# Optimization experiments

Hardware: AMD Instinct MI355X
Metric: run time of the kernel (lower is better)

Reference implementation:

```python
import jax, jax.numpy as jnp
import numpy as np

T, H, NH, NKV, HD = 2048, 1024, 16, 4, 64
I, E, TOPK = 2048, 8, 2
EPS = 1e-5
ROPE_BASE = 10000.0


def rms_norm(x, w):
    var = jnp.mean(x * x, axis=-1, keepdims=True)
    return x * jax.lax.rsqrt(var + EPS) * w


def apply_rope(x, positions, n_heads):
    # neox-style rotary over full head_dim
    t = x.reshape(-1, n_heads, HD)
    half = HD // 2
    inv_freq = 1.0 / (ROPE_BASE ** (jnp.arange(0, half, dtype=jnp.float32) / half))
    freqs = positions.astype(jnp.float32)[:, None] * inv_freq[None, :]  # [T, half]
    cos = jnp.cos(freqs)[:, None, :]
    sin = jnp.sin(freqs)[:, None, :]
    x1, x2 = t[..., :half], t[..., half:]
    rot = jnp.concatenate([x1 * cos - x2 * sin, x2 * cos + x1 * sin], axis=-1)
    return rot.reshape(x.shape)


def setup_inputs():
    key = jax.random.key(0)
    ks = jax.random.split(key, 9)
    s = 0.02
    return dict(
        positions=jnp.arange(T, dtype=jnp.int32),
        hidden_states=jax.random.normal(ks[0], (T, H), jnp.float32),
        input_ln_w=jnp.ones((H,), jnp.float32),
        post_ln_w=jnp.ones((H,), jnp.float32),
        residual_ln_w=jnp.ones((H,), jnp.float32),
        qkv_w=jax.random.normal(ks[1], ((NH + 2 * NKV) * HD, H), jnp.float32) * s,
        o_w=jax.random.normal(ks[2], (H, NH * HD), jnp.float32) * s,
        gate_w=jax.random.normal(ks[3], (E, H), jnp.float32) * s,
        ws=jax.random.normal(ks[4], (E, 2 * I, H), jnp.float32) * s,
        w2s=jax.random.normal(ks[5], (E, H, I), jnp.float32) * s,
        res_w13=jax.random.normal(ks[6], (2 * H, H), jnp.float32) * s,
        res_w2=jax.random.normal(ks[7], (H, H), jnp.float32) * s,
    )


def attention(x, positions, qkv_w, o_w):
    qkv = x @ qkv_w.T  # [T, (NH+2*NKV)*HD]
    q, k, v = jnp.split(qkv, [NH * HD, NH * HD + NKV * HD], axis=-1)
    q = apply_rope(q, positions, NH)
    k = apply_rope(k, positions, NKV)
    q = q.reshape(T, NH, HD)
    k = k.reshape(T, NKV, HD)
    v = v.reshape(T, NKV, HD)
    rep = NH // NKV  # GQA: repeat kv heads
    k = jnp.repeat(k, rep, axis=1)
    v = jnp.repeat(v, rep, axis=1)
    scale = HD ** -0.5
    scores = jnp.einsum('tnd,snd->nts', q, k) * scale  # [NH, T, T]
    causal = jnp.tril(jnp.ones((T, T), dtype=bool))
    scores = jnp.where(causal[None], scores, -jnp.inf)
    probs = jax.nn.softmax(scores, axis=-1)
    out = jnp.einsum('nts,snd->tnd', probs, v).reshape(T, NH * HD)
    return out @ o_w.T


def silu_and_mul(gu):
    g, u = jnp.split(gu, 2, axis=-1)
    return jax.nn.silu(g) * u


def moe(x, gate_w, ws, w2s):
    logits = x @ gate_w.T  # [T, E]
    probs = jax.nn.softmax(logits, axis=-1)
    topk_w, topk_ids = jax.lax.top_k(probs, TOPK)
    topk_w = topk_w / jnp.sum(topk_w, axis=-1, keepdims=True)  # renormalize (top_k > 1)
    routes = jnp.zeros((x.shape[0], E), x.dtype).at[
        jnp.arange(x.shape[0])[:, None], topk_ids].set(topk_w)  # [T, E] sparse routing
    gu = jnp.einsum('th,eih->tei', x, ws)        # [T, E, 2I]
    act = silu_and_mul(gu)                        # [T, E, I]
    eo = jnp.einsum('tei,ehi->teh', act, w2s)     # [T, E, H]
    return jnp.einsum('te,teh->th', routes, eo)


def reference(positions, hidden_states, input_ln_w, post_ln_w, residual_ln_w,
              qkv_w, o_w, gate_w, ws, w2s, res_w13, res_w2):
    residual_input = hidden_states
    h = rms_norm(hidden_states, input_ln_w)
    h = attention(h, positions, qkv_w, o_w)
    residual_attn = residual_input + h
    # parallel residual MLP branch (ffn_dim == hidden)
    r = rms_norm(residual_attn, residual_ln_w)
    r = silu_and_mul(r @ res_w13.T) @ res_w2.T
    residual_mlp = residual_attn + r
    # MoE branch
    m = rms_norm(residual_attn, post_ln_w)
    m = moe(m, gate_w, ws, w2s)
    return residual_mlp + m
```

## Files before the change

kernel.cpp:

```cpp
#include <hip/hip_runtime.h>
#include <stdint.h>


typedef _Float16 f16;
typedef _Float16 f16x8 __attribute__((ext_vector_type(8)));
typedef _Float16 f16x4 __attribute__((ext_vector_type(4)));
typedef float f32x4 __attribute__((ext_vector_type(4)));

#define DEV __device__ __forceinline__

DEV void glds16(const void* g, void* l) {
  __builtin_amdgcn_global_load_lds((const __attribute__((address_space(1))) void*)g,
                                   (__attribute__((address_space(3))) void*)l, 16, 0, 0);
}

__global__ void cvt_f16_kernel(const float* __restrict__ in, f16* __restrict__ outp) {
  const size_t i = ((size_t)blockIdx.x * 256 + threadIdx.x) * 4;
  float4 f = *(const float4*)(in + i);
  f16x4 o;
  o[0] = (f16)f.x; o[1] = (f16)f.y; o[2] = (f16)f.z; o[3] = (f16)f.w;
  *(f16x4*)(outp + i) = o;
}

__global__ void cvt_f16x2_kernel(const float* __restrict__ in,
                                 f16* __restrict__ oh, f16* __restrict__ ol) {
  const size_t i = ((size_t)blockIdx.x * 256 + threadIdx.x) * 4;
  float4 f = *(const float4*)(in + i);
  f16x4 h, l;
  h[0] = (f16)f.x; l[0] = (f16)(f.x - (float)h[0]);
  h[1] = (f16)f.y; l[1] = (f16)(f.y - (float)h[1]);
  h[2] = (f16)f.z; l[2] = (f16)(f.z - (float)h[2]);
  h[3] = (f16)f.w; l[3] = (f16)(f.w - (float)h[3]);
  *(f16x4*)(oh + i) = h;
  *(f16x4*)(ol + i) = l;
}

__global__ void rmsnorm_kernel(const float* __restrict__ in, const float* __restrict__ w,
                               f16* __restrict__ outp) {
  const int t = blockIdx.x * 4 + (threadIdx.x >> 6);
  const int lane = threadIdx.x & 63;
  const float* x = in + (size_t)t * 1024;
  float v[16]; float ss = 0.f;
#pragma unroll
  for (int j = 0; j < 16; j++) { float a = x[lane + 64 * j]; v[j] = a; ss += a * a; }
#pragma unroll
  for (int m = 1; m < 64; m <<= 1) ss += __shfl_xor(ss, m);
  const float rs = rsqrtf(ss * (1.f / 1024.f) + 1e-5f);
#pragma unroll
  for (int j = 0; j < 16; j++)
    outp[(size_t)t * 1024 + lane + 64 * j] = (f16)(v[j] * rs * w[lane + 64 * j]);
}

__global__ void rmsnorm_dual_kernel(const float* __restrict__ in,
                                    const float* __restrict__ w1, const float* __restrict__ w2,
                                    f16* __restrict__ o1, f16* __restrict__ o2) {
  const int t = blockIdx.x * 4 + (threadIdx.x >> 6);
  const int lane = threadIdx.x & 63;
  const float* x = in + (size_t)t * 1024;
  float v[16]; float ss = 0.f;
#pragma unroll
  for (int j = 0; j < 16; j++) { float a = x[lane + 64 * j]; v[j] = a; ss += a * a; }
#pragma unroll
  for (int m = 1; m < 64; m <<= 1) ss += __shfl_xor(ss, m);
  const float rs = rsqrtf(ss * (1.f / 1024.f) + 1e-5f);
#pragma unroll
  for (int j = 0; j < 16; j++) {
    float nv = v[j] * rs;
    size_t idx = (size_t)t * 1024 + lane + 64 * j;
    o1[idx] = (f16)(nv * w1[lane + 64 * j]);
    o2[idx] = (f16)(nv * w2[lane + 64 * j]);
  }
}

template <int EPI, int BN, int SPLITK = 1>
__global__ __launch_bounds__(256) void gemm_f16_kernel(
    const f16* __restrict__ A, const f16* __restrict__ B,
    void* __restrict__ outp, const float* __restrict__ addsrc,
    int M, int N, int K) {
  constexpr int JT = BN / 32;
  constexpr int L = (BN == 128) ? 4 : 3;
  __shared__ __attribute__((aligned(16))) f16 As[4][128 * 32];
  __shared__ __attribute__((aligned(16))) f16 Bs[4][BN * 32];
  const int tid = threadIdx.x;
  const size_t row0 = (size_t)blockIdx.y * 128, col0 = (size_t)blockIdx.x * BN;
  const int ks = (SPLITK > 1) ? (int)blockIdx.z : 0;
  const int kspan = K / SPLITK, kb = ks * kspan;
  const int nt = kspan >> 5;
  const int c0 = tid, c1 = tid + 256;
  const int sw0 = ((c0 & 3) ^ ((c0 >> 3) & 3)) * 8;
  const int sw1 = ((c1 & 3) ^ ((c1 >> 3) & 3)) * 8;
  const f16* a0 = A + (row0 + (c0 >> 2)) * K + sw0;
  const f16* a1 = A + (row0 + (c1 >> 2)) * K + sw1;
  const f16* b0 = B + (col0 + (c0 >> 2)) * K + sw0;
  const f16* b1 = B + (col0 + ((BN == 128) ? (c1 >> 2) : 0)) * K + ((BN == 128) ? sw1 : 0);

  const int wave = tid >> 6, lane = tid & 63, lr = lane >> 4, lc = lane & 15;
  const int wr = wave >> 1, wc = wave & 1;
  const int rsw = (lr ^ ((lc >> 1) & 3)) * 8;

  f32x4 acc[4][JT];
#pragma unroll
  for (int i = 0; i < 4; i++)
#pragma unroll
    for (int j = 0; j < JT; j++) acc[i][j] = (f32x4){0.f, 0.f, 0.f, 0.f};

  auto stage = [&](int k0, int buf) {
    glds16(a0 + k0, As[buf] + c0 * 8);
    glds16(a1 + k0, As[buf] + c1 * 8);
    glds16(b0 + k0, Bs[buf] + c0 * 8);
    if constexpr (BN == 128) glds16(b1 + k0, Bs[buf] + c1 * 8);
  };

  stage(kb, 0); stage(kb + 32, 1); stage(kb + 64, 2);
  for (int t = 0; t < nt; ++t) {
    if (t <= nt - 3)      asm volatile("s_waitcnt vmcnt(%0)" :: "n"(2 * L) : "memory");
    else if (t == nt - 2) asm volatile("s_waitcnt vmcnt(%0)" :: "n"(L) : "memory");
    else                  asm volatile("s_waitcnt vmcnt(0)" ::: "memory");
    __builtin_amdgcn_s_barrier();
    asm volatile("" ::: "memory");
    if (t + 3 < nt) stage(kb + (t + 3) * 32, (t + 3) & 3);
    const f16* Ab = As[t & 3];
    const f16* Bb = Bs[t & 3];
    f16x8 af[4], bfr[JT];
#pragma unroll
    for (int i = 0; i < 4; i++)
      af[i] = *(const f16x8*)(Ab + (wr * 64 + i * 16 + lc) * 32 + rsw);
#pragma unroll
    for (int j = 0; j < JT; j++)
      bfr[j] = *(const f16x8*)(Bb + (wc * (BN / 2) + j * 16 + lc) * 32 + rsw);
#pragma unroll
    for (int i = 0; i < 4; i++)
#pragma unroll
      for (int j = 0; j < JT; j++)
        acc[i][j] = __builtin_amdgcn_mfma_f32_16x16x32_f16(af[i], bfr[j], acc[i][j], 0, 0, 0);
  }

#pragma unroll
  for (int i = 0; i < 4; i++)
#pragma unroll
    for (int j = 0; j < JT; j++) {
      const size_t rbase = row0 + wr * 64 + i * 16 + lr * 4;
      const size_t col = col0 + wc * (BN / 2) + j * 16 + lc;
#pragma unroll
      for (int r = 0; r < 4; r++) {
        size_t idx = (rbase + r) * N + col;
        if constexpr (SPLITK > 1) {
          ((float*)outp)[(size_t)ks * M * N + idx] = acc[i][j][r];
        } else if constexpr (EPI == 0) ((float*)outp)[idx] = acc[i][j][r];
        else if constexpr (EPI == 1) ((float*)outp)[idx] = acc[i][j][r] + addsrc[idx];
        else ((f16*)outp)[idx] = (f16)acc[i][j][r];
      }
    }
}

template <int SPLITK>
__global__ __launch_bounds__(256) void gemm_f16x2_add_kernel(
    const f16* __restrict__ Ah, const f16* __restrict__ Al,
    const f16* __restrict__ Bh, const f16* __restrict__ Bl,
    float* __restrict__ outp, const float* __restrict__ addsrc,
    int M, int N, int K) {
  __shared__ __attribute__((aligned(16))) f16 Ash[3][128 * 32];
  __shared__ __attribute__((aligned(16))) f16 Asl[3][128 * 32];
  __shared__ __attribute__((aligned(16))) f16 Bsh[3][64 * 32];
  __shared__ __attribute__((aligned(16))) f16 Bsl[3][64 * 32];
  const int tid = threadIdx.x;
  const size_t row0 = (size_t)blockIdx.y * 128, col0 = (size_t)blockIdx.x * 64;
  const int ks = (SPLITK > 1) ? (int)blockIdx.z : 0;
  const int kspan = K / SPLITK, kb = ks * kspan;
  const int nt = kspan >> 5;
  const int c0 = tid, c1 = tid + 256;
  const int sw0 = ((c0 & 3) ^ ((c0 >> 3) & 3)) * 8;
  const int sw1 = ((c1 & 3) ^ ((c1 >> 3) & 3)) * 8;
  const size_t aoff0 = (row0 + (c0 >> 2)) * K + sw0;
  const size_t aoff1 = (row0 + (c1 >> 2)) * K + sw1;
  const size_t boff0 = (col0 + (c0 >> 2)) * K + sw0;

  const int wave = tid >> 6, lane = tid & 63, lr = lane >> 4, lc = lane & 15;
  const int wr = wave >> 1, wc = wave & 1;
  const int rsw = (lr ^ ((lc >> 1) & 3)) * 8;

  f32x4 acc[4][2];
#pragma unroll
  for (int i = 0; i < 4; i++)
#pragma unroll
    for (int j = 0; j < 2; j++) acc[i][j] = (f32x4){0.f, 0.f, 0.f, 0.f};

  auto stage = [&](int k0, int buf) {
    glds16(Ah + aoff0 + k0, Ash[buf] + c0 * 8);
    glds16(Ah + aoff1 + k0, Ash[buf] + c1 * 8);
    glds16(Al + aoff0 + k0, Asl[buf] + c0 * 8);
    glds16(Al + aoff1 + k0, Asl[buf] + c1 * 8);
    glds16(Bh + boff0 + k0, Bsh[buf] + c0 * 8);
    glds16(Bl + boff0 + k0, Bsl[buf] + c0 * 8);
  };

  stage(kb, 0); stage(kb + 32, 1);
  int bc = 0, bs = 2;
  for (int t = 0; t < nt; ++t) {
    if (t <= nt - 2) asm volatile("s_waitcnt vmcnt(%0)" :: "n"(6) : "memory");
    else             asm volatile("s_waitcnt vmcnt(0)" ::: "memory");
    __builtin_amdgcn_s_barrier();
    asm volatile("" ::: "memory");
    if (t + 2 < nt) stage(kb + (t + 2) * 32, bs);
    f16x8 afh[4], afl[4], bfh[2], bfl[2];
#pragma unroll
    for (int i = 0; i < 4; i++) {
      const int ro = (wr * 64 + i * 16 + lc) * 32 + rsw;
      afh[i] = *(const f16x8*)(Ash[bc] + ro);
      afl[i] = *(const f16x8*)(Asl[bc] + ro);
    }
#pragma unroll
    for (int j = 0; j < 2; j++) {
      const int ro = (wc * 32 + j * 16 + lc) * 32 + rsw;
      bfh[j] = *(const f16x8*)(Bsh[bc] + ro);
      bfl[j] = *(const f16x8*)(Bsl[bc] + ro);
    }
#pragma unroll
    for (int i = 0; i < 4; i++)
#pragma unroll
      for (int j = 0; j < 2; j++) {
        acc[i][j] = __builtin_amdgcn_mfma_f32_16x16x32_f16(afh[i], bfh[j], acc[i][j], 0, 0, 0);
        acc[i][j] = __builtin_amdgcn_mfma_f32_16x16x32_f16(afh[i], bfl[j], acc[i][j], 0, 0, 0);
        acc[i][j] = __builtin_amdgcn_mfma_f32_16x16x32_f16(afl[i], bfh[j], acc[i][j], 0, 0, 0);
      }
    bc = (bc == 2) ? 0 : bc + 1;
    bs = (bs == 2) ? 0 : bs + 1;
  }

#pragma unroll
  for (int i = 0; i < 4; i++)
#pragma unroll
    for (int j = 0; j < 2; j++) {
      const size_t rbase = row0 + wr * 64 + i * 16 + lr * 4;
      const size_t col = col0 + wc * 32 + j * 16 + lc;
#pragma unroll
      for (int r = 0; r < 4; r++) {
        size_t idx = (rbase + r) * N + col;
        if constexpr (SPLITK > 1) outp[(size_t)ks * M * N + idx] = acc[i][j][r];
        else outp[idx] = acc[i][j][r] + addsrc[idx];
      }
    }
}

template <int DIVROW, int BN, int SPLITK = 1>
__global__ __launch_bounds__(256) void gemm_moe_kernel(
    const f16* __restrict__ A, const f16* __restrict__ Ball, void* __restrict__ outp,
    const int* __restrict__ perm, const int* __restrict__ counts,
    int N, int K, size_t strideB) {
  constexpr int JT = BN / 32;
  constexpr int L = (BN == 128) ? 4 : 3;
  const int e = (int)blockIdx.z / SPLITK;
  const int ks = (int)blockIdx.z % SPLITK;
  const int cnt = counts[e];
  const int bm = blockIdx.y;
  if (bm * 128 >= cnt) return;
  const int kspan = K / SPLITK, kb = ks * kspan;
  const int nt = kspan >> 5;
  const f16* B = Ball + (size_t)e * strideB;
  __shared__ __attribute__((aligned(16))) f16 As[4][128 * 32];
  __shared__ __attribute__((aligned(16))) f16 Bs[4][BN * 32];
  const int tid = threadIdx.x;
  const size_t col0 = (size_t)blockIdx.x * BN;
  const int c0 = tid, c1 = tid + 256;
  const int pbase = e * 2048 + bm * 128;
  const int rt0 = c0 >> 2, rt1 = c1 >> 2;
  const int sid0 = (bm * 128 + rt0 < cnt) ? perm[pbase + rt0] : 0;
  const int sid1 = (bm * 128 + rt1 < cnt) ? perm[pbase + rt1] : 0;
  const size_t ar0 = DIVROW ? (size_t)(sid0 >> 1) : (size_t)sid0;
  const size_t ar1 = DIVROW ? (size_t)(sid1 >> 1) : (size_t)sid1;
  const int sw0 = ((c0 & 3) ^ ((c0 >> 3) & 3)) * 8;
  const int sw1 = ((c1 & 3) ^ ((c1 >> 3) & 3)) * 8;
  const f16* ap0 = A + ar0 * K + sw0;
  const f16* ap1 = A + ar1 * K + sw1;
  const f16* b0 = B + (col0 + (c0 >> 2)) * K + sw0;
  const f16* b1 = B + (col0 + ((BN == 128) ? (c1 >> 2) : 0)) * K + ((BN == 128) ? sw1 : 0);

  const int wave = tid >> 6, lane = tid & 63, lr = lane >> 4, lc = lane & 15;
  const int wr = wave >> 1, wc = wave & 1;
  const int rsw = (lr ^ ((lc >> 1) & 3)) * 8;

  f32x4 acc[4][JT];
#pragma unroll
  for (int i = 0; i < 4; i++)
#pragma unroll
    for (int j = 0; j < JT; j++) acc[i][j] = (f32x4){0.f, 0.f, 0.f, 0.f};

  auto stage = [&](int k0, int buf) {
    glds16(ap0 + k0, As[buf] + c0 * 8);
    glds16(ap1 + k0, As[buf] + c1 * 8);
    glds16(b0 + k0, Bs[buf] + c0 * 8);
    if constexpr (BN == 128) glds16(b1 + k0, Bs[buf] + c1 * 8);
  };

  stage(kb, 0); stage(kb + 32, 1); stage(kb + 64, 2);
  for (int t = 0; t < nt; ++t) {
    if (t <= nt - 3)      asm volatile("s_waitcnt vmcnt(%0)" :: "n"(2 * L) : "memory");
    else if (t == nt - 2) asm volatile("s_waitcnt vmcnt(%0)" :: "n"(L) : "memory");
    else                  asm volatile("s_waitcnt vmcnt(0)" ::: "memory");
    __builtin_amdgcn_s_barrier();
    asm volatile("" ::: "memory");
    if (t + 3 < nt) stage(kb + (t + 3) * 32, (t + 3) & 3);
    const f16* Ab = As[t & 3];
    const f16* Bb = Bs[t & 3];
    f16x8 af[4], bfr[JT];
#pragma unroll
    for (int i = 0; i < 4; i++)
      af[i] = *(const f16x8*)(Ab + (wr * 64 + i * 16 + lc) * 32 + rsw);
#pragma unroll
    for (int j = 0; j < JT; j++)
      bfr[j] = *(const f16x8*)(Bb + (wc * (BN / 2) + j * 16 + lc) * 32 + rsw);
#pragma unroll
    for (int i = 0; i < 4; i++)
#pragma unroll
      for (int j = 0; j < JT; j++)
        acc[i][j] = __builtin_amdgcn_mfma_f32_16x16x32_f16(af[i], bfr[j], acc[i][j], 0, 0, 0);
  }

  int sids[4][4];
#pragma unroll
  for (int i = 0; i < 4; i++)
#pragma unroll
    for (int r = 0; r < 4; r++) {
      int rit = wr * 64 + i * 16 + lr * 4 + r;
      sids[i][r] = (bm * 128 + rit < cnt) ? perm[pbase + rit] : -1;
    }
#pragma unroll
  for (int i = 0; i < 4; i++)
#pragma unroll
    for (int j = 0; j < JT; j++) {
      const size_t col = col0 + wc * (BN / 2) + j * 16 + lc;
#pragma unroll
      for (int r = 0; r < 4; r++)
        if (sids[i][r] >= 0) {
          if constexpr (SPLITK > 1)
            ((float*)outp)[((size_t)ks * 4096 + sids[i][r]) * N + col] = acc[i][j][r];
          else
            ((f16*)outp)[(size_t)sids[i][r] * N + col] = (f16)acc[i][j][r];
        }
    }
}

__global__ void rope_kernel(const float* __restrict__ qkv, const int* __restrict__ pos,
                            f16* __restrict__ qr, f16* __restrict__ kr) {
  const int t = blockIdx.y;
  const int u = blockIdx.x * 256 + threadIdx.x;
  if (u >= 640) return;
  const float* b0 = qkv + (size_t)t * 1536;
  const float* b1 = b0 + (size_t)2048 * 1536;
  const int head = u >> 5, i = u & 31;
  const bool isq = head < 16;
  const int off = isq ? head * 64 + i : 1024 + (head - 16) * 64 + i;
  const float x1 = b0[off] + b1[off], x2 = b0[off + 32] + b1[off + 32];
  const double ph = (double)pos[t] * exp((double)i * -0.28782313662425575);
  const float c = (float)cos(ph), s = (float)sin(ph);
  const float r1 = x1 * c - x2 * s, r2 = x2 * c + x1 * s;
  if (isq) {
    const float qs = 0.18033688011116042f;
    qr[(size_t)t * 1024 + head * 64 + i] = (f16)(qs * r1);
    qr[(size_t)t * 1024 + head * 64 + i + 32] = (f16)(qs * r2);
  } else {
    const int kh = head - 16;
    kr[(size_t)t * 256 + kh * 64 + i] = (f16)r1;
    kr[(size_t)t * 256 + kh * 64 + i + 32] = (f16)r2;
  }
}

__global__ void vtrans_kernel(const float* __restrict__ qkvf, f16* __restrict__ vt) {
  __shared__ float Ts[64 * 69];
  const int t0 = blockIdx.x * 64;
  const int kv = blockIdx.y;
  const int tid = threadIdx.x;
  const int tr = tid >> 2, jj = tid & 3;
  const float* src0 = qkvf + (size_t)(t0 + tr) * 1536 + 1280 + kv * 64 + jj * 16;
  const float* src1 = src0 + (size_t)2048 * 1536;
#pragma unroll
  for (int x = 0; x < 4; x++) {
    float4 f = *(const float4*)(src0 + x * 4);
    float4 g = *(const float4*)(src1 + x * 4);
    Ts[tr * 69 + jj * 16 + x * 4 + 0] = f.x + g.x;
    Ts[tr * 69 + jj * 16 + x * 4 + 1] = f.y + g.y;
    Ts[tr * 69 + jj * 16 + x * 4 + 2] = f.z + g.z;
    Ts[tr * 69 + jj * 16 + x * 4 + 3] = f.w + g.w;
  }
  __syncthreads();
  f16* dst = vt + (size_t)(kv * 64 + tr) * 2048 + t0 + jj * 16;
#pragma unroll
  for (int x = 0; x < 2; x++) {
    f16x8 o;
#pragma unroll
    for (int i = 0; i < 8; i++) o[i] = (f16)Ts[(jj * 16 + x * 8 + i) * 69 + tr];
    *(f16x8*)(dst + x * 8) = o;
  }
}

__global__ void add3_kernel(float* __restrict__ o, const float* __restrict__ a,
                            const float* __restrict__ p0, const float* __restrict__ p1) {
  const size_t i4 = ((size_t)blockIdx.x * 256 + threadIdx.x) * 4;
  float4 va = *(const float4*)(a + i4);
  float4 v0 = *(const float4*)(p0 + i4);
  float4 v1 = *(const float4*)(p1 + i4);
  va.x += v0.x + v1.x;
  va.y += v0.y + v1.y;
  va.z += v0.z + v1.z;
  va.w += v0.w + v1.w;
  *(float4*)(o + i4) = va;
}

__global__ __launch_bounds__(256, 3) void attn_kernel(
    const f16* __restrict__ qr, const f16* __restrict__ kr, const f16* __restrict__ vt,
    f16* __restrict__ ahi, f16* __restrict__ alo) {
  const int qt = 31 - (int)blockIdx.x;
  const int h = blockIdx.y;
  const int kvh = h >> 2;
  __shared__ __attribute__((aligned(16))) f16 Ks[128 * 72];
  __shared__ __attribute__((aligned(16))) f16 Vs[64 * 136];
  __shared__ __attribute__((aligned(16))) f16 Pl[4 * 16 * 136];
  const int tid = threadIdx.x;
  const int wave = tid >> 6, lane = tid & 63, lr = lane >> 4, lc = lane & 15;
  const int trow = qt * 64 + wave * 16 + lc;
  f16* Pw = Pl + wave * 16 * 136;

  const int krow = tid >> 3, kcol = (tid & 7) * 8;
  const int vrow = tid >> 4, vcol = (tid & 15) * 8;
  const f16* kgbase = kr + (size_t)kvh * 64 + kcol;
  const f16* vgbase = vt + (size_t)(kvh * 64 + vrow) * 2048 + vcol;

  const f16* qp = qr + (size_t)trow * 1024 + h * 64 + lr * 8;
  f16x8 qf0 = *(const f16x8*)(qp);
  f16x8 qf1 = *(const f16x8*)(qp + 32);

  float m_run = -3e38f, l_run = 0.f;
  f32x4 accO[4];
#pragma unroll
  for (int jo = 0; jo < 4; jo++) accO[jo] = (f32x4){0.f, 0.f, 0.f, 0.f};

  const int nch = (qt >> 1) + 1;

  f16x8 kreg[4], vreg[4];
#pragma unroll
  for (int it = 0; it < 4; it++) {
    kreg[it] = *(const f16x8*)(kgbase + (size_t)(it * 32 + krow) * 256);
    vreg[it] = *(const f16x8*)(vgbase + it * 16 * 2048);
  }

  for (int ch = 0; ch < nch; ++ch) {
    const int c0 = ch * 128;
    const bool last = (ch == nch - 1);

    __syncthreads();
#pragma unroll
    for (int it = 0; it < 4; it++) {
      *(f16x8*)(Ks + (it * 32 + krow) * 72 + kcol) = kreg[it];
      *(f16x8*)(Vs + (it * 16 + vrow) * 136 + vcol) = vreg[it];
    }
    __syncthreads();

    if (!last) {
      const int c1 = c0 + 128;
#pragma unroll
      for (int it = 0; it < 4; it++) {
        kreg[it] = *(const f16x8*)(kgbase + (size_t)(c1 + it * 32 + krow) * 256);
        vreg[it] = *(const f16x8*)(vgbase + it * 16 * 2048 + c1);
      }
    }

    f32x4 st[8];
#pragma unroll
    for (int j = 0; j < 8; j++) {
      const f16* kp = Ks + (j * 16 + lc) * 72 + lr * 8;
      f16x8 ka0 = *(const f16x8*)(kp);
      f16x8 ka1 = *(const f16x8*)(kp + 32);
      f32x4 s = (f32x4){0.f, 0.f, 0.f, 0.f};
      s = __builtin_amdgcn_mfma_f32_16x16x32_f16(ka0, qf0, s, 0, 0, 0);
      s = __builtin_amdgcn_mfma_f32_16x16x32_f16(ka1, qf1, s, 0, 0, 0);
      st[j] = s;
    }

    if (last) {
#pragma unroll
      for (int j = 0; j < 8; j++)
#pragma unroll
        for (int r = 0; r < 4; r++)
          if (c0 + j * 16 + lr * 4 + r > trow) st[j][r] = -3e38f;
    }

    float mc = -3e38f;
#pragma unroll
    for (int j = 0; j < 8; j++)
      mc = fmaxf(mc, fmaxf(fmaxf(st[j][0], st[j][1]), fmaxf(st[j][2], st[j][3])));
    mc = fmaxf(mc, __shfl_xor(mc, 16));
    mc = fmaxf(mc, __shfl_xor(mc, 32));
    const float mn = fmaxf(m_run, mc);
    const float alpha = __builtin_amdgcn_exp2f(m_run - mn);
    m_run = mn;

    float ls = 0.f;
#pragma unroll
    for (int j = 0; j < 8; j++) {
      f16x4 pv;
#pragma unroll
      for (int r = 0; r < 4; r++) {
        float e = __builtin_amdgcn_exp2f(st[j][r] - mn);
        ls += e;
        pv[r] = (f16)e;
      }
      *(f16x4*)(Pw + lc * 136 + j * 16 + lr * 4) = pv;
    }
    ls += __shfl_xor(ls, 16);
    ls += __shfl_xor(ls, 32);
    l_run = l_run * alpha + ls;
#pragma unroll
    for (int jo = 0; jo < 4; jo++) accO[jo] *= alpha;

#pragma unroll
    for (int kkt = 0; kkt < 4; kkt++) {
      f16x8 pb = *(const f16x8*)(Pw + lc * 136 + kkt * 32 + lr * 8);
#pragma unroll
      for (int jo = 0; jo < 4; jo++) {
        f16x8 va = *(const f16x8*)(Vs + (jo * 16 + lc) * 136 + kkt * 32 + lr * 8);
        accO[jo] = __builtin_amdgcn_mfma_f32_16x16x32_f16(va, pb, accO[jo], 0, 0, 0);
      }
    }
  }

  const float inv = 1.f / l_run;
#pragma unroll
  for (int jo = 0; jo < 4; jo++) {
    f16x4 hi4, lo4;
#pragma unroll
    for (int r = 0; r < 4; r++) {
      float o = accO[jo][r] * inv;
      f16 hv = (f16)o;
      hi4[r] = hv;
      lo4[r] = (f16)(o - (float)hv);
    }
    const size_t idx = (size_t)trow * 1024 + h * 64 + jo * 16 + lr * 4;
    *(f16x4*)(ahi + idx) = hi4;
    *(f16x4*)(alo + idx) = lo4;
  }
}

__global__ void routing_kernel(const float* __restrict__ resA,
                               const float* __restrict__ postw,
                               const float* __restrict__ gw,
                               int* __restrict__ counts, int* __restrict__ perm,
                               float* __restrict__ rw) {
  const int t = blockIdx.x * 4 + (threadIdx.x >> 6);
  const int lane = threadIdx.x & 63;
  const float* x = resA + (size_t)t * 1024;
  float v[16]; float ss = 0.f;
#pragma unroll
  for (int j = 0; j < 16; j++) { float a = x[lane + 64 * j]; v[j] = a; ss += a * a; }
#pragma unroll
  for (int m = 1; m < 64; m <<= 1) ss += __shfl_xor(ss, m);
  const float rs = rsqrtf(ss * (1.f / 1024.f) + 1e-5f);
#pragma unroll
  for (int j = 0; j < 16; j++) v[j] *= rs * postw[lane + 64 * j];
  float lg[8];
#pragma unroll
  for (int e = 0; e < 8; e++) {
    float p = 0.f;
    const float* g = gw + (size_t)e * 1024;
#pragma unroll
    for (int j = 0; j < 16; j++) p += v[j] * g[lane + 64 * j];
#pragma unroll
    for (int m = 1; m < 64; m <<= 1) p += __shfl_xor(p, m);
    lg[e] = p;
  }
  if (lane == 0) {
    int e0 = 0; float b0 = lg[0];
#pragma unroll
    for (int e = 1; e < 8; e++) if (lg[e] > b0) { b0 = lg[e]; e0 = e; }
    int e1 = -1; float b1 = -3e38f;
#pragma unroll
    for (int e = 0; e < 8; e++) if (e != e0 && lg[e] > b1) { b1 = lg[e]; e1 = e; }
    const float w0 = 1.f / (1.f + expf(b1 - b0));
    const float w1 = 1.f - w0;
    int p0 = atomicAdd(&counts[e0], 1);
    perm[e0 * 2048 + p0] = t * 2;
    int p1 = atomicAdd(&counts[e1], 1);
    perm[e1 * 2048 + p1] = t * 2 + 1;
    rw[t * 2] = w0;
    rw[t * 2 + 1] = w1;
  }
}

__global__ void silu_mul_kernel(const f16* __restrict__ gu, f16* __restrict__ outp, int lgN) {
  const int N = 1 << lgN;
  const size_t i4 = ((size_t)blockIdx.x * 256 + threadIdx.x) * 4;
  const size_t r = i4 >> lgN;
  const int c = (int)(i4 & (N - 1));
  const f16* gp = gu + r * (size_t)(2 * N) + c;
  f16x4 g = *(const f16x4*)gp;
  f16x4 u = *(const f16x4*)(gp + N);
  f16x4 o;
#pragma unroll
  for (int x = 0; x < 4; x++) {
    float gg = (float)g[x], uu = (float)u[x];
    o[x] = (f16)(gg / (1.f + __expf(-gg)) * uu);
  }
  *(f16x4*)(outp + r * (size_t)N + c) = o;
}

__global__ void final_add4_kernel(float* __restrict__ outp, const float* __restrict__ eo4,
                                  const float* __restrict__ rw) {
  const size_t i4 = ((size_t)blockIdx.x * 256 + threadIdx.x) * 4;
  const int t = (int)(i4 >> 10);
  const int c = (int)(i4 & 1023);
  const float w0 = rw[2 * t], w1 = rw[2 * t + 1];
  float4 s0 = {0.f, 0.f, 0.f, 0.f}, s1 = {0.f, 0.f, 0.f, 0.f};
#pragma unroll
  for (int ks = 0; ks < 4; ks++) {
    const float* p = eo4 + (size_t)ks * 4096 * 1024;
    float4 a = *(const float4*)(p + (size_t)(2 * t) * 1024 + c);
    float4 b = *(const float4*)(p + (size_t)(2 * t + 1) * 1024 + c);
    s0.x += a.x; s0.y += a.y; s0.z += a.z; s0.w += a.w;
    s1.x += b.x; s1.y += b.y; s1.z += b.z; s1.w += b.w;
  }
  float4 o = *(float4*)(outp + i4);
  o.x += w0 * s0.x + w1 * s1.x;
  o.y += w0 * s0.y + w1 * s1.y;
  o.z += w0 * s0.z + w1 * s1.z;
  o.w += w0 * s0.w + w1 * s1.w;
  *(float4*)(outp + i4) = o;
}

extern "C" void kernel_launch(void* const* d_in, const int* in_sizes, int n_in,
                              void* d_out, int out_size, void* d_ws, size_t ws_size,
                              hipStream_t stream) {
  const int* positions = (const int*)d_in[0];
  const float* hidden = (const float*)d_in[1];
  const float* in_ln = (const float*)d_in[2];
  const float* post_ln = (const float*)d_in[3];
  const float* res_ln = (const float*)d_in[4];
  const float* qkv_w = (const float*)d_in[5];
  const float* o_w = (const float*)d_in[6];
  const float* gate_w = (const float*)d_in[7];
  const float* ws_w = (const float*)d_in[8];
  const float* w2s_w = (const float*)d_in[9];
  const float* w13_w = (const float*)d_in[10];
  const float* w2_w = (const float*)d_in[11];
  float* out = (float*)d_out;

  char* p = (char*)d_ws;
  auto alloc = [&](size_t b) { void* r = (void*)p; p += (b + 255) & ~(size_t)255; return r; };

  f16* wqkv = (f16*)alloc((size_t)1536 * 1024 * 2);
  f16* woh  = (f16*)alloc((size_t)1024 * 1024 * 2);
  f16* wol  = (f16*)alloc((size_t)1024 * 1024 * 2);
  f16* wws  = (f16*)alloc((size_t)8 * 4096 * 1024 * 2);
  f16* ww2  = (f16*)alloc((size_t)8 * 1024 * 2048 * 2);
  f16* w13  = (f16*)alloc((size_t)2048 * 1024 * 2);
  f16* w2c  = (f16*)alloc((size_t)1024 * 1024 * 2);
  f16* hn   = (f16*)alloc((size_t)2048 * 1024 * 2);
  float* qkvp = (float*)alloc((size_t)2 * 2048 * 1536 * 4);
  f16* qr = (f16*)alloc((size_t)2048 * 1024 * 2);
  f16* kr = (f16*)alloc((size_t)2048 * 256 * 2);
  f16* vt = (f16*)alloc((size_t)256 * 2048 * 2);
  f16* ath = (f16*)alloc((size_t)2048 * 1024 * 2);
  f16* atl = (f16*)alloc((size_t)2048 * 1024 * 2);
  float* opp = (float*)alloc((size_t)2 * 2048 * 1024 * 4);
  float* resA = (float*)alloc((size_t)2048 * 1024 * 4);
  f16* rn = (f16*)alloc((size_t)2048 * 1024 * 2);
  f16* mn = (f16*)alloc((size_t)2048 * 1024 * 2);
  f16* gu13 = (f16*)alloc((size_t)2048 * 2048 * 2);
  f16* act13 = (f16*)alloc((size_t)2048 * 1024 * 2);
  float* w2p = (float*)alloc((size_t)2 * 2048 * 1024 * 4);
  f16* gum = (f16*)alloc((size_t)4096 * 4096 * 2);
  f16* actm = (f16*)alloc((size_t)4096 * 2048 * 2);
  float* eo4 = (float*)alloc((size_t)4 * 4096 * 1024 * 4);
  float* rw = (float*)alloc((size_t)4096 * 4);
  int* counts = (int*)alloc(256);
  int* perm = (int*)alloc((size_t)8 * 2048 * 4);

  cvt_f16_kernel<<<dim3(1536 * 1024 / 1024), dim3(256), 0, stream>>>(qkv_w, wqkv);
  cvt_f16_kernel<<<dim3(8 * 4096 * 1024 / 1024), dim3(256), 0, stream>>>(ws_w, wws);
  cvt_f16_kernel<<<dim3(8 * 1024 * 2048 / 1024), dim3(256), 0, stream>>>(w2s_w, ww2);
  cvt_f16_kernel<<<dim3(2048 * 1024 / 1024), dim3(256), 0, stream>>>(w13_w, w13);
  cvt_f16_kernel<<<dim3(1024 * 1024 / 1024), dim3(256), 0, stream>>>(w2_w, w2c);
  cvt_f16x2_kernel<<<dim3(1024 * 1024 / 1024), dim3(256), 0, stream>>>(o_w, woh, wol);
  hipMemsetAsync(counts, 0, 256, stream);

  rmsnorm_kernel<<<dim3(512), dim3(256), 0, stream>>>(hidden, in_ln, hn);
  gemm_f16_kernel<0, 64, 2><<<dim3(24, 16, 2), dim3(256), 0, stream>>>(
      hn, wqkv, (void*)qkvp, (const float*)nullptr, 2048, 1536, 1024);
  rope_kernel<<<dim3(3, 2048), dim3(256), 0, stream>>>(qkvp, positions, qr, kr);
  vtrans_kernel<<<dim3(32, 4), dim3(256), 0, stream>>>(qkvp, vt);
  attn_kernel<<<dim3(32, 16), dim3(256), 0, stream>>>(qr, kr, vt, ath, atl);
  gemm_f16x2_add_kernel<2><<<dim3(16, 16, 2), dim3(256), 0, stream>>>(
      ath, atl, woh, wol, opp, (const float*)nullptr, 2048, 1024, 1024);
  add3_kernel<<<dim3(2048), dim3(256), 0, stream>>>(
      resA, hidden, opp, opp + (size_t)2048 * 1024);

  rmsnorm_dual_kernel<<<dim3(512), dim3(256), 0, stream>>>(resA, res_ln, post_ln, rn, mn);
  routing_kernel<<<dim3(512), dim3(256), 0, stream>>>(resA, post_ln, gate_w, counts, perm, rw);

  gemm_f16_kernel<2, 64><<<dim3(32, 16), dim3(256), 0, stream>>>(
      rn, w13, (void*)gu13, (const float*)nullptr, 2048, 2048, 1024);
  silu_mul_kernel<<<dim3(2048 * 1024 / 1024), dim3(256), 0, stream>>>(gu13, act13, 10);
  gemm_f16_kernel<0, 64, 2><<<dim3(16, 16, 2), dim3(256), 0, stream>>>(
      act13, w2c, (void*)w2p, (const float*)nullptr, 2048, 1024, 1024);
  add3_kernel<<<dim3(2048), dim3(256), 0, stream>>>(
      out, resA, w2p, w2p + (size_t)2048 * 1024);

  gemm_moe_kernel<1, 128><<<dim3(32, 16, 8), dim3(256), 0, stream>>>(
      mn, wws, (void*)gum, perm, counts, 4096, 1024, (size_t)4096 * 1024);
  silu_mul_kernel<<<dim3(4096 * 2048 / 1024), dim3(256), 0, stream>>>(gum, actm, 11);
  gemm_moe_kernel<0, 128, 4><<<dim3(8, 16, 32), dim3(256), 0, stream>>>(
      actm, ww2, (void*)eo4, perm, counts, 1024, 2048, (size_t)1024 * 2048);
  final_add4_kernel<<<dim3(2048 * 1024 / 1024), dim3(256), 0, stream>>>(out, eo4, rw);
}
```

Measured before the change: 650.3 us.

## Shrink GEMM pipelines to triple buffering, precompute RoPE table, halve MoE split-K

The f16 and MoE GEMM kernels drop from four LDS buffers with three-stage prefetch to three buffers with two-stage prefetch, and the f16x2 kernel's buffer indexing becomes t%3. This lowers shared memory per block so more blocks can be resident, at the cost of less latency hiding. RoPE cos/sin are now computed once per (position, frequency) in a separate table kernel instead of in double precision for every head. The MoE down-projection uses split-K 2 instead of 4, which halves the partial-sum buffer and the reduction traffic in the final add but launches fewer blocks.

```diff
diff --git a/kernel.cpp b/kernel.cpp
--- a/kernel.cpp
+++ b/kernel.cpp
@@ -79,8 +79,8 @@
     int M, int N, int K) {
   constexpr int JT = BN / 32;
   constexpr int L = (BN == 128) ? 4 : 3;
-  __shared__ __attribute__((aligned(16))) f16 As[4][128 * 32];
-  __shared__ __attribute__((aligned(16))) f16 Bs[4][BN * 32];
+  __shared__ __attribute__((aligned(16))) f16 As[3][128 * 32];
+  __shared__ __attribute__((aligned(16))) f16 Bs[3][BN * 32];
   const int tid = threadIdx.x;
   const size_t row0 = (size_t)blockIdx.y * 128, col0 = (size_t)blockIdx.x * BN;
   const int ks = (SPLITK > 1) ? (int)blockIdx.z : 0;
@@ -111,16 +111,15 @@
     if constexpr (BN == 128) glds16(b1 + k0, Bs[buf] + c1 * 8);
   };
 
-  stage(kb, 0); stage(kb + 32, 1); stage(kb + 64, 2);
+  stage(kb, 0); stage(kb + 32, 1);
   for (int t = 0; t < nt; ++t) {
-    if (t <= nt - 3)      asm volatile("s_waitcnt vmcnt(%0)" :: "n"(2 * L) : "memory");
-    else if (t == nt - 2) asm volatile("s_waitcnt vmcnt(%0)" :: "n"(L) : "memory");
-    else                  asm volatile("s_waitcnt vmcnt(0)" ::: "memory");
+    if (t < nt - 1) asm volatile("s_waitcnt vmcnt(%0)" :: "n"(L) : "memory");
+    else            asm volatile("s_waitcnt vmcnt(0)" ::: "memory");
     __builtin_amdgcn_s_barrier();
     asm volatile("" ::: "memory");
-    if (t + 3 < nt) stage(kb + (t + 3) * 32, (t + 3) & 3);
-    const f16* Ab = As[t & 3];
-    const f16* Bb = Bs[t & 3];
+    if (t + 2 < nt) stage(kb + (t + 2) * 32, (t + 2) % 3);
+    const f16* Ab = As[t % 3];
+    const f16* Bb = Bs[t % 3];
     f16x8 af[4], bfr[JT];
 #pragma unroll
     for (int i = 0; i < 4; i++)
@@ -195,13 +194,13 @@
   };
 
   stage(kb, 0); stage(kb + 32, 1);
-  int bc = 0, bs = 2;
   for (int t = 0; t < nt; ++t) {
-    if (t <= nt - 2) asm volatile("s_waitcnt vmcnt(%0)" :: "n"(6) : "memory");
-    else             asm volatile("s_waitcnt vmcnt(0)" ::: "memory");
+    if (t < nt - 1) asm volatile("s_waitcnt vmcnt(%0)" :: "n"(6) : "memory");
+    else            asm volatile("s_waitcnt vmcnt(0)" ::: "memory");
     __builtin_amdgcn_s_barrier();
     asm volatile("" ::: "memory");
-    if (t + 2 < nt) stage(kb + (t + 2) * 32, bs);
+    if (t + 2 < nt) stage(kb + (t + 2) * 32, (t + 2) % 3);
+    const int bc = t % 3;
     f16x8 afh[4], afl[4], bfh[2], bfl[2];
 #pragma unroll
     for (int i = 0; i < 4; i++) {
@@ -223,8 +222,6 @@
         acc[i][j] = __builtin_amdgcn_mfma_f32_16x16x32_f16(afh[i], bfl[j], acc[i][j], 0, 0, 0);
         acc[i][j] = __builtin_amdgcn_mfma_f32_16x16x32_f16(afl[i], bfh[j], acc[i][j], 0, 0, 0);
       }
-    bc = (bc == 2) ? 0 : bc + 1;
-    bs = (bs == 2) ? 0 : bs + 1;
   }
 
 #pragma unroll
@@ -257,8 +254,8 @@
   const int kspan = K / SPLITK, kb = ks * kspan;
   const int nt = kspan >> 5;
   const f16* B = Ball + (size_t)e * strideB;
-  __shared__ __attribute__((aligned(16))) f16 As[4][128 * 32];
-  __shared__ __attribute__((aligned(16))) f16 Bs[4][BN * 32];
+  __shared__ __attribute__((aligned(16))) f16 As[3][128 * 32];
+  __shared__ __attribute__((aligned(16))) f16 Bs[3][BN * 32];
   const int tid = threadIdx.x;
   const size_t col0 = (size_t)blockIdx.x * BN;
   const int c0 = tid, c1 = tid + 256;
@@ -292,16 +289,15 @@
     if constexpr (BN == 128) glds16(b1 + k0, Bs[buf] + c1 * 8);
   };
 
-  stage(kb, 0); stage(kb + 32, 1); stage(kb + 64, 2);
+  stage(kb, 0); stage(kb + 32, 1);
   for (int t = 0; t < nt; ++t) {
-    if (t <= nt - 3)      asm volatile("s_waitcnt vmcnt(%0)" :: "n"(2 * L) : "memory");
-    else if (t == nt - 2) asm volatile("s_waitcnt vmcnt(%0)" :: "n"(L) : "memory");
-    else                  asm volatile("s_waitcnt vmcnt(0)" ::: "memory");
+    if (t < nt - 1) asm volatile("s_waitcnt vmcnt(%0)" :: "n"(L) : "memory");
+    else            asm volatile("s_waitcnt vmcnt(0)" ::: "memory");
     __builtin_amdgcn_s_barrier();
     asm volatile("" ::: "memory");
-    if (t + 3 < nt) stage(kb + (t + 3) * 32, (t + 3) & 3);
-    const f16* Ab = As[t & 3];
-    const f16* Bb = Bs[t & 3];
+    if (t + 2 < nt) stage(kb + (t + 2) * 32, (t + 2) % 3);
+    const f16* Ab = As[t % 3];
+    const f16* Bb = Bs[t % 3];
     f16x8 af[4], bfr[JT];
 #pragma unroll
     for (int i = 0; i < 4; i++)
@@ -340,7 +336,14 @@
     }
 }
 
-__global__ void rope_kernel(const float* __restrict__ qkv, const int* __restrict__ pos,
+__global__ void rope_table_kernel(const int* __restrict__ pos, float2* __restrict__ tab) {
+  const int idx = blockIdx.x * 256 + threadIdx.x;
+  const int t = idx >> 5, i = idx & 31;
+  const double ph = (double)pos[t] * exp((double)i * -0.28782313662425575);
+  tab[idx] = make_float2((float)cos(ph), (float)sin(ph));
+}
+
+__global__ void rope_kernel(const float* __restrict__ qkv, const float2* __restrict__ tab,
                             f16* __restrict__ qr, f16* __restrict__ kr) {
   const int t = blockIdx.y;
   const int u = blockIdx.x * 256 + threadIdx.x;
@@ -351,8 +354,8 @@
   const bool isq = head < 16;
   const int off = isq ? head * 64 + i : 1024 + (head - 16) * 64 + i;
   const float x1 = b0[off] + b1[off], x2 = b0[off + 32] + b1[off + 32];
-  const double ph = (double)pos[t] * exp((double)i * -0.28782313662425575);
-  const float c = (float)cos(ph), s = (float)sin(ph);
+  const float2 cs = tab[t * 32 + i];
+  const float c = cs.x, s = cs.y;
   const float r1 = x1 * c - x2 * s, r2 = x2 * c + x1 * s;
   if (isq) {
     const float qs = 0.18033688011116042f;
@@ -602,7 +605,7 @@
   *(f16x4*)(outp + r * (size_t)N + c) = o;
 }
 
-__global__ void final_add4_kernel(float* __restrict__ outp, const float* __restrict__ eo4,
+__global__ void final_add2_kernel(float* __restrict__ outp, const float* __restrict__ eo2,
                                   const float* __restrict__ rw) {
   const size_t i4 = ((size_t)blockIdx.x * 256 + threadIdx.x) * 4;
   const int t = (int)(i4 >> 10);
@@ -610,8 +613,8 @@
   const float w0 = rw[2 * t], w1 = rw[2 * t + 1];
   float4 s0 = {0.f, 0.f, 0.f, 0.f}, s1 = {0.f, 0.f, 0.f, 0.f};
 #pragma unroll
-  for (int ks = 0; ks < 4; ks++) {
-    const float* p = eo4 + (size_t)ks * 4096 * 1024;
+  for (int ks = 0; ks < 2; ks++) {
+    const float* p = eo2 + (size_t)ks * 4096 * 1024;
     float4 a = *(const float4*)(p + (size_t)(2 * t) * 1024 + c);
     float4 b = *(const float4*)(p + (size_t)(2 * t + 1) * 1024 + c);
     s0.x += a.x; s0.y += a.y; s0.z += a.z; s0.w += a.w;
@@ -654,6 +657,7 @@
   f16* w2c  = (f16*)alloc((size_t)1024 * 1024 * 2);
   f16* hn   = (f16*)alloc((size_t)2048 * 1024 * 2);
   float* qkvp = (float*)alloc((size_t)2 * 2048 * 1536 * 4);
+  float2* ptab = (float2*)alloc((size_t)2048 * 32 * 8);
   f16* qr = (f16*)alloc((size_t)2048 * 1024 * 2);
   f16* kr = (f16*)alloc((size_t)2048 * 256 * 2);
   f16* vt = (f16*)alloc((size_t)256 * 2048 * 2);
@@ -668,7 +672,7 @@
   float* w2p = (float*)alloc((size_t)2 * 2048 * 1024 * 4);
   f16* gum = (f16*)alloc((size_t)4096 * 4096 * 2);
   f16* actm = (f16*)alloc((size_t)4096 * 2048 * 2);
-  float* eo4 = (float*)alloc((size_t)4 * 4096 * 1024 * 4);
+  float* eo2 = (float*)alloc((size_t)2 * 4096 * 1024 * 4);
   float* rw = (float*)alloc((size_t)4096 * 4);
   int* counts = (int*)alloc(256);
   int* perm = (int*)alloc((size_t)8 * 2048 * 4);
@@ -679,12 +683,13 @@
   cvt_f16_kernel<<<dim3(2048 * 1024 / 1024), dim3(256), 0, stream>>>(w13_w, w13);
   cvt_f16_kernel<<<dim3(1024 * 1024 / 1024), dim3(256), 0, stream>>>(w2_w, w2c);
   cvt_f16x2_kernel<<<dim3(1024 * 1024 / 1024), dim3(256), 0, stream>>>(o_w, woh, wol);
+  rope_table_kernel<<<dim3(256), dim3(256), 0, stream>>>(positions, ptab);
   hipMemsetAsync(counts, 0, 256, stream);
 
   rmsnorm_kernel<<<dim3(512), dim3(256), 0, stream>>>(hidden, in_ln, hn);
   gemm_f16_kernel<0, 64, 2><<<dim3(24, 16, 2), dim3(256), 0, stream>>>(
       hn, wqkv, (void*)qkvp, (const float*)nullptr, 2048, 1536, 1024);
-  rope_kernel<<<dim3(3, 2048), dim3(256), 0, stream>>>(qkvp, positions, qr, kr);
+  rope_kernel<<<dim3(3, 2048), dim3(256), 0, stream>>>(qkvp, ptab, qr, kr);
   vtrans_kernel<<<dim3(32, 4), dim3(256), 0, stream>>>(qkvp, vt);
   attn_kernel<<<dim3(32, 16), dim3(256), 0, stream>>>(qr, kr, vt, ath, atl);
   gemm_f16x2_add_kernel<2><<<dim3(16, 16, 2), dim3(256), 0, stream>>>(
@@ -706,7 +711,7 @@
   gemm_moe_kernel<1, 128><<<dim3(32, 16, 8), dim3(256), 0, stream>>>(
       mn, wws, (void*)gum, perm, counts, 4096, 1024, (size_t)4096 * 1024);
   silu_mul_kernel<<<dim3(4096 * 2048 / 1024), dim3(256), 0, stream>>>(gum, actm, 11);
-  gemm_moe_kernel<0, 128, 4><<<dim3(8, 16, 32), dim3(256), 0, stream>>>(
-      actm, ww2, (void*)eo4, perm, counts, 1024, 2048, (size_t)1024 * 2048);
-  final_add4_kernel<<<dim3(2048 * 1024 / 1024), dim3(256), 0, stream>>>(out, eo4, rw);
-}
+  gemm_moe_kernel<0, 128, 2><<<dim3(8, 16, 16), dim3(256), 0, stream>>>(
+      actm, ww2, (void*)eo2, perm, counts, 1024, 2048, (size_t)1024 * 2048);
+  final_add2_kernel<<<dim3(2048 * 1024 / 1024), dim3(256), 0, stream>>>(out, eo2, rw);
+}
```

After: 622.2 us. -4.3%, faster.
